# Kernel tuning notes

Hardware: AMD Instinct MI355X
Metric: run time of the kernel (lower is better)

The kernel has to match this reference:

```python
import jax, jax.numpy as jnp
import numpy as np

N_HEADS = 8
TOPK = 64
LN_EPS = 1e-5


def layernorm(x, g, b):
    mu = jnp.mean(x, axis=-1, keepdims=True)
    var = jnp.mean((x - mu) ** 2, axis=-1, keepdims=True)
    return (x - mu) * jax.lax.rsqrt(var + LN_EPS) * g + b


def mha(x, wq, wk, wv, wo, causal):
    # x: [B, S, H]; weights are torch nn.Linear style [out, in]
    B, S, H = x.shape
    hd = H // N_HEADS
    scale = 1.0 / np.sqrt(hd)

    def proj(w):
        return (x @ w.T).reshape(B, S, N_HEADS, hd).transpose(0, 2, 1, 3)  # [B, n, S, hd]

    q, k, v = proj(wq), proj(wk), proj(wv)
    s = jnp.einsum('bnqd,bnkd->bnqk', q, k) * scale
    if causal:
        m = jnp.tril(jnp.ones((S, S), bool))
        s = jnp.where(m, s, jnp.finfo(s.dtype).min)
    a = jax.nn.softmax(s, axis=-1)
    o = jnp.einsum('bnqk,bnkd->bnqd', a, v).transpose(0, 2, 1, 3).reshape(B, S, H)
    return o @ wo.T


def topk_activation(x, k):
    # x: [N, F]; keep top-k per row, zero elsewhere (matches topk + scatter_)
    vals, idx = jax.lax.top_k(x, k)
    rows = jnp.arange(x.shape[0])[:, None]
    return jnp.zeros_like(x).at[rows, idx].set(vals)


def setup_inputs() -> dict:
    key = jax.random.key(0)
    B, D, L, H, F = 8, 16, 128, 512, 4096
    ks = jax.random.split(key, 12)
    s = 1.0 / np.sqrt(H)
    w = lambda k, shp, sc: jax.random.normal(k, shp, jnp.float32) * sc
    return {
        'zL': w(ks[0], (B, D, L, H), 1.0),
        'wq_l': w(ks[1], (H, H), s), 'wk_l': w(ks[2], (H, H), s),
        'wv_l': w(ks[3], (H, H), s), 'wo_l': w(ks[4], (H, H), s),
        'gamma_l': jnp.ones(H, jnp.float32), 'beta_l': jnp.zeros(H, jnp.float32),
        'wq_d': w(ks[5], (H, H), s), 'wk_d': w(ks[6], (H, H), s),
        'wv_d': w(ks[7], (H, H), s), 'wo_d': w(ks[8], (H, H), s),
        'gamma_d': jnp.ones(H, jnp.float32), 'beta_d': jnp.zeros(H, jnp.float32),
        'dict_enc': w(ks[9], (F, H), np.sqrt(2.0 / (H + F))),
        'bias_pre': jnp.zeros(H, jnp.float32),
        'bias_enc': jnp.zeros(F, jnp.float32),
        'query_token': jnp.zeros(H, jnp.float32),
    }


def reference(zL, wq_l, wk_l, wv_l, wo_l, gamma_l, beta_l,
              wq_d, wk_d, wv_d, wo_d, gamma_d, beta_d,
              dict_enc, bias_pre, bias_enc, query_token):
    B, D, L, H = zL.shape
    F = dict_enc.shape[0]
    # prepend learned query token along depth, drop last layer
    qt = jnp.broadcast_to(query_token[None, None, None, :], (B, 1, L, H))
    x = jnp.concatenate([qt, zL[:, :-1, :, :]], axis=1)  # [B, D, L, H]
    # non-causal attention over L within each (b, d)
    x = x.reshape(B * D, L, H)
    x = x + mha(layernorm(x, gamma_l, beta_l), wq_l, wk_l, wv_l, wo_l, causal=False)
    # causal attention over D within each (b, l)
    x = x.reshape(B, D, L, H).transpose(0, 2, 1, 3).reshape(B * L, D, H)
    x = x + mha(layernorm(x, gamma_d, beta_d), wq_d, wk_d, wv_d, wo_d, causal=True)
    x_prior = x.reshape(B, L, D, H).transpose(0, 2, 1, 3)  # [B, D, L, H]
    # dictionary encode on residual (detached in original)
    N = B * D * L
    x_src = jax.lax.stop_gradient(zL - x_prior).reshape(N, H)
    logits = (x_src - bias_pre[None, :]) @ dict_enc.T + bias_enc
    z_dense = jax.nn.relu(logits)
    z_flat = topk_activation(z_dense, TOPK)
    z_n = z_flat.reshape(B, D, L, F)
    return z_n, x_prior
```

## Files before the change

kernel.cpp:

```cpp
#include <hip/hip_runtime.h>
#include <stdint.h>

#define NTOK 16384
#define HDIM 512
#define FDIM 4096
#define NHEAD 8

typedef __attribute__((ext_vector_type(8))) _Float16 f16x8;
typedef __attribute__((ext_vector_type(16))) float f32x16;
#define LOSCALE 4096.0f
#define LOINV   (1.0f / 4096.0f)

static __device__ __forceinline__ void ld8f(const float* p, float* v) {
    *(float4*)&v[0] = *(const float4*)p;
    *(float4*)&v[4] = *(const float4*)(p + 4);
}
static __device__ __forceinline__ void st8f(float* p, const float* v) {
    *(float4*)p       = *(const float4*)&v[0];
    *(float4*)(p + 4) = *(const float4*)&v[4];
}

__global__ __launch_bounds__(256) void build_x_k(const float* __restrict__ zL,
                                                 const float* __restrict__ qt,
                                                 float* __restrict__ X) {
    int idx = blockIdx.x * 256 + threadIdx.x;
    int n = idx >> 6;
    int h = (idx & 63) << 3;
    int d = (n >> 7) & 15;
    const float* src = d ? (zL + (((size_t)(n - 128)) << 9) + h) : (qt + h);
    float v[8];
    ld8f(src, v);
    st8f(X + (((size_t)n) << 9) + h, v);
}

__global__ __launch_bounds__(256) void ln_stats_k(const float* __restrict__ X,
                                                  float* __restrict__ mu,
                                                  float* __restrict__ rstd) {
    int row = blockIdx.x * 4 + (threadIdx.x >> 6);
    int lane = threadIdx.x & 63;
    const float* xr = X + (((size_t)row) << 9) + (lane << 3);
    float v[8];
    ld8f(xr, v);
    float s = 0.f;
#pragma unroll
    for (int i = 0; i < 8; ++i) s += v[i];
#pragma unroll
    for (int off = 32; off; off >>= 1) s += __shfl_xor(s, off);
    float m = s * (1.0f / 512.0f);
    float q = 0.f;
#pragma unroll
    for (int i = 0; i < 8; ++i) { float d = v[i] - m; q += d * d; }
#pragma unroll
    for (int off = 32; off; off >>= 1) q += __shfl_xor(q, off);
    if (lane == 0) {
        mu[row] = m;
        rstd[row] = 1.0f / sqrtf(q * (1.0f / 512.0f) + 1e-5f);
    }
}

template<bool LN, bool ADD_C, bool BIAS>
__global__ __launch_bounds__(256) void gemm_k(const float* __restrict__ A,
                                              const float* __restrict__ W,
                                              float* __restrict__ C,
                                              const float* __restrict__ mu,
                                              const float* __restrict__ rstd,
                                              const float* __restrict__ gamma,
                                              const float* __restrict__ beta,
                                              const float* __restrict__ bias,
                                              int M, int N, int K) {
    __shared__ float As[16][128];
    __shared__ float Bs[16][128];
    const int tid = threadIdx.x;
    const int bm = blockIdx.y << 7;
    const int bn = blockIdx.x << 7;
    const int tx = tid & 15, ty = tid >> 4;
    const int lr = tid >> 1;
    const int lk = (tid & 1) << 3;
    const float* Ap = A + (size_t)(bm + lr) * K + lk;
    const float* Wp = W + (size_t)(bn + lr) * K + lk;
    float mu_r = 0.f, rs_r = 0.f;
    if (LN) { mu_r = mu[bm + lr]; rs_r = rstd[bm + lr]; }
    float acc[8][8];
#pragma unroll
    for (int i = 0; i < 8; ++i)
#pragma unroll
        for (int j = 0; j < 8; ++j) acc[i][j] = 0.f;

    float av[8], bv[8];
    ld8f(Ap, av);
    ld8f(Wp, bv);
    if (LN) {
        float gv[8], be[8];
        ld8f(gamma + lk, gv);
        ld8f(beta + lk, be);
#pragma unroll
        for (int i = 0; i < 8; ++i) av[i] = (av[i] - mu_r) * rs_r * gv[i] + be[i];
    }
    const int nIt = K >> 4;
    for (int it = 0; it < nIt; ++it) {
        __syncthreads();
#pragma unroll
        for (int i = 0; i < 8; ++i) { As[lk + i][lr] = av[i]; Bs[lk + i][lr] = bv[i]; }
        __syncthreads();
        if (it + 1 < nIt) {
            const int k0 = (it + 1) << 4;
            ld8f(Ap + k0, av);
            ld8f(Wp + k0, bv);
            if (LN) {
                float gv[8], be[8];
                ld8f(gamma + k0 + lk, gv);
                ld8f(beta + k0 + lk, be);
#pragma unroll
                for (int i = 0; i < 8; ++i) av[i] = (av[i] - mu_r) * rs_r * gv[i] + be[i];
            }
        }
#pragma unroll
        for (int kk = 0; kk < 16; ++kk) {
            float a[8], b[8];
            *(float4*)&a[0] = *(const float4*)&As[kk][ty << 3];
            *(float4*)&a[4] = *(const float4*)&As[kk][(ty << 3) + 4];
            *(float4*)&b[0] = *(const float4*)&Bs[kk][tx << 3];
            *(float4*)&b[4] = *(const float4*)&Bs[kk][(tx << 3) + 4];
#pragma unroll
            for (int i = 0; i < 8; ++i)
#pragma unroll
                for (int j = 0; j < 8; ++j)
                    acc[i][j] = fmaf(a[i], b[j], acc[i][j]);
        }
    }
    const int orow = bm + (ty << 3);
    const int ocol = bn + (tx << 3);
    float badd[8];
    if (BIAS) ld8f(bias + ocol, badd);
#pragma unroll
    for (int i = 0; i < 8; ++i) {
        float* cp = C + (size_t)(orow + i) * N + ocol;
        float o[8];
#pragma unroll
        for (int j = 0; j < 8; ++j) o[j] = acc[i][j];
        if (BIAS) {
#pragma unroll
            for (int j = 0; j < 8; ++j) o[j] += badd[j];
        }
        if (ADD_C) {
            float4 c0 = *(const float4*)cp;
            float4 c1 = *(const float4*)(cp + 4);
            o[0] += c0.x; o[1] += c0.y; o[2] += c0.z; o[3] += c0.w;
            o[4] += c1.x; o[5] += c1.y; o[6] += c1.z; o[7] += c1.w;
        }
        *(float4*)cp       = make_float4(o[0], o[1], o[2], o[3]);
        *(float4*)(cp + 4) = make_float4(o[4], o[5], o[6], o[7]);
    }
}

__global__ __launch_bounds__(512) void attn_l_k(float* __restrict__ QO,
                                                const float* __restrict__ K,
                                                const float* __restrict__ V) {
    __shared__ float ks[128][64];
    __shared__ float vs[128][64];
    const int seq = blockIdx.x, head = blockIdx.y;
    const int t = threadIdx.x;
    const size_t base = (((size_t)seq) << 16) + (head << 6);
#pragma unroll
    for (int i = 0; i < 4; ++i) {
        int slot = t + (i << 9);
        int row = slot >> 4;
        int c4 = (slot & 15) << 2;
        size_t g = base + (((size_t)row) << 9) + c4;
        *(float4*)&ks[row][c4] = *(const float4*)(K + g);
        *(float4*)&vs[row][c4] = *(const float4*)(V + g);
    }
    __syncthreads();
    const int r = t >> 2;
    const int q16 = (t & 3) << 4;
    float* qp = QO + base + (((size_t)r) << 9) + q16;
    float qr[16];
#pragma unroll
    for (int i = 0; i < 4; ++i) *(float4*)&qr[i << 2] = *(const float4*)(qp + (i << 2));
    float o[16];
#pragma unroll
    for (int d = 0; d < 16; ++d) o[d] = 0.f;
    float m = -1e30f, l = 0.f;
    for (int j = 0; j < 128; ++j) {
        const float* kp = &ks[j][q16];
        float s0 = 0.f, s1 = 0.f, s2 = 0.f, s3 = 0.f;
#pragma unroll
        for (int d = 0; d < 16; d += 4) {
            s0 = fmaf(qr[d + 0], kp[d + 0], s0);
            s1 = fmaf(qr[d + 1], kp[d + 1], s1);
            s2 = fmaf(qr[d + 2], kp[d + 2], s2);
            s3 = fmaf(qr[d + 3], kp[d + 3], s3);
        }
        float sp = (s0 + s1) + (s2 + s3);
        sp += __shfl_xor(sp, 1);
        sp += __shfl_xor(sp, 2);
        float s = sp * 0.125f;
        if (s > m) {
            float c = expf(m - s);
#pragma unroll
            for (int d = 0; d < 16; ++d) o[d] *= c;
            l *= c;
            m = s;
        }
        float w = expf(s - m);
        l += w;
        const float* vp = &vs[j][q16];
#pragma unroll
        for (int d = 0; d < 16; ++d) o[d] = fmaf(w, vp[d], o[d]);
    }
    float inv = 1.0f / l;
#pragma unroll
    for (int i = 0; i < 4; ++i)
        *(float4*)(qp + (i << 2)) = make_float4(o[i * 4] * inv, o[i * 4 + 1] * inv,
                                                o[i * 4 + 2] * inv, o[i * 4 + 3] * inv);
}

__global__ __launch_bounds__(128) void attn_d_k(float* __restrict__ QO,
                                                const float* __restrict__ K,
                                                const float* __restrict__ V) {
    __shared__ float ks[16][512];
    __shared__ float vs[16][512];
    const int bl = blockIdx.x;
    const int b = bl >> 7, l = bl & 127;
    const int t = threadIdx.x;
    const size_t base = ((size_t)(b * 2048 + l)) << 9;
#pragma unroll
    for (int i = 0; i < 16; ++i) {
        int slot = t + (i << 7);
        int row = slot >> 7;
        int c4 = (slot & 127) << 2;
        size_t g = base + (((size_t)row) << 16) + c4;
        *(float4*)&ks[row][c4] = *(const float4*)(K + g);
        *(float4*)&vs[row][c4] = *(const float4*)(V + g);
    }
    __syncthreads();
    const int head = t >> 4, dr = t & 15;
    const int ho = head << 6;
    float qr[64];
    float* qp = QO + base + (((size_t)dr) << 16) + ho;
#pragma unroll
    for (int i = 0; i < 16; ++i) *(float4*)&qr[i << 2] = *(const float4*)(qp + (i << 2));
    float s[16];
    float m = -1e30f;
#pragma unroll
    for (int j = 0; j < 16; ++j) {
        float s0 = 0.f, s1 = 0.f, s2 = 0.f, s3 = 0.f;
#pragma unroll
        for (int d = 0; d < 64; d += 4) {
            s0 = fmaf(qr[d + 0], ks[j][ho + d + 0], s0);
            s1 = fmaf(qr[d + 1], ks[j][ho + d + 1], s1);
            s2 = fmaf(qr[d + 2], ks[j][ho + d + 2], s2);
            s3 = fmaf(qr[d + 3], ks[j][ho + d + 3], s3);
        }
        float sv = ((s0 + s1) + (s2 + s3)) * 0.125f;
        s[j] = (j <= dr) ? sv : -1e30f;
        m = fmaxf(m, s[j]);
    }
    float lsum = 0.f;
#pragma unroll
    for (int j = 0; j < 16; ++j) {
        float w = (j <= dr) ? expf(s[j] - m) : 0.f;
        s[j] = w;
        lsum += w;
    }
    float inv = 1.0f / lsum;
    float o[64];
#pragma unroll
    for (int d = 0; d < 64; ++d) o[d] = 0.f;
#pragma unroll
    for (int j = 0; j < 16; ++j) {
        float w = s[j];
#pragma unroll
        for (int d = 0; d < 64; ++d) o[d] = fmaf(w, vs[j][ho + d], o[d]);
    }
#pragma unroll
    for (int i = 0; i < 16; ++i)
        *(float4*)(qp + (i << 2)) = make_float4(o[i * 4] * inv, o[i * 4 + 1] * inv,
                                                o[i * 4 + 2] * inv, o[i * 4 + 3] * inv);
}

__global__ __launch_bounds__(256) void cast_out_k(const float* __restrict__ X,
                                                  float* __restrict__ out) {
    int idx = blockIdx.x * 256 + threadIdx.x;
    float v[8];
    ld8f(X + (((size_t)idx) << 3), v);
    st8f(out + (((size_t)idx) << 3), v);
}

__global__ __launch_bounds__(256) void xsrc_k(const float* __restrict__ zL,
                                              const float* __restrict__ bias_pre,
                                              float* __restrict__ X) {
    int idx = blockIdx.x * 256 + threadIdx.x;
    int h = (idx & 63) << 3;
    float z[8], p[8], x[8];
    ld8f(zL + (((size_t)idx) << 3), z);
    ld8f(bias_pre + h, p);
    float* xp = X + (((size_t)idx) << 3);
    ld8f(xp, x);
    float o[8];
#pragma unroll
    for (int i = 0; i < 8; ++i) o[i] = z[i] - x[i] - p[i];
    st8f(xp, o);
}

__global__ __launch_bounds__(256) void xprior_xsrc_k(const float* __restrict__ zL,
                                                     const float* __restrict__ bias_pre,
                                                     float* __restrict__ X,
                                                     float* __restrict__ out_xp) {
    int idx = blockIdx.x * 256 + threadIdx.x;
    int h = (idx & 63) << 3;
    float z[8], p[8], x[8];
    ld8f(zL + (((size_t)idx) << 3), z);
    ld8f(bias_pre + h, p);
    float* xp = X + (((size_t)idx) << 3);
    ld8f(xp, x);
    st8f(out_xp + (((size_t)idx) << 3), x);
    float o[8];
#pragma unroll
    for (int i = 0; i < 8; ++i) o[i] = z[i] - x[i] - p[i];
    st8f(xp, o);
}

__global__ __launch_bounds__(256) void split2_k(const float* __restrict__ in,
                                                _Float16* __restrict__ ph,
                                                _Float16* __restrict__ pl) {
    int idx = blockIdx.x * 256 + threadIdx.x;
    float v[8];
    ld8f(in + (((size_t)idx) << 3), v);
    _Float16 h8[8], l8[8];
#pragma unroll
    for (int i = 0; i < 8; ++i) {
        _Float16 h = (_Float16)v[i];
        float r = v[i] - (float)h;
        h8[i] = h;
        l8[i] = (_Float16)(r * LOSCALE);
    }
    *(int4*)(ph + (((size_t)idx) << 3)) = *(int4*)h8;
    *(int4*)(pl + (((size_t)idx) << 3)) = *(int4*)l8;
}

__global__ __launch_bounds__(256) void split2_ln_k(const float* __restrict__ X,
                                                   const float* __restrict__ mu,
                                                   const float* __restrict__ rstd,
                                                   const float* __restrict__ gamma,
                                                   const float* __restrict__ beta,
                                                   _Float16* __restrict__ ph,
                                                   _Float16* __restrict__ pl) {
    int idx = blockIdx.x * 256 + threadIdx.x;
    int row = idx >> 6;
    int h = (idx & 63) << 3;
    float v[8], gv[8], be[8];
    ld8f(X + (((size_t)idx) << 3), v);
    ld8f(gamma + h, gv);
    ld8f(beta + h, be);
    float m = mu[row], rs = rstd[row];
    _Float16 h8[8], l8[8];
#pragma unroll
    for (int i = 0; i < 8; ++i) {
        float y = (v[i] - m) * rs * gv[i] + be[i];
        _Float16 hh = (_Float16)y;
        float r = y - (float)hh;
        h8[i] = hh;
        l8[i] = (_Float16)(r * LOSCALE);
    }
    *(int4*)(ph + (((size_t)idx) << 3)) = *(int4*)h8;
    *(int4*)(pl + (((size_t)idx) << 3)) = *(int4*)l8;
}

#define LDT 36
template<bool ADD_C, bool BIAS>
__global__ __launch_bounds__(256) void gemm_f16_k(
        const _Float16* __restrict__ Xh, const _Float16* __restrict__ Xl,
        const _Float16* __restrict__ Wh, const _Float16* __restrict__ Wl,
        const float* __restrict__ bias, float* __restrict__ Cout, int ldc) {
    __shared__ _Float16 Ah[128][LDT], Al[128][LDT];
    __shared__ _Float16 Bh[128][LDT], Bl[128][LDT];
    const int tid = threadIdx.x;
    const int bm = blockIdx.y << 7, bn = blockIdx.x << 7;
    const int w = tid >> 6, lane = tid & 63;
    const int wr = w >> 1, wc = w & 1;
    const int l31 = lane & 31, hh = lane >> 5;
    f32x16 acc1[2][2], acc2[2][2];
#pragma unroll
    for (int i = 0; i < 2; ++i)
#pragma unroll
        for (int j = 0; j < 2; ++j)
#pragma unroll
            for (int r = 0; r < 16; ++r) { acc1[i][j][r] = 0.f; acc2[i][j][r] = 0.f; }

    for (int k0 = 0; k0 < HDIM; k0 += 32) {
        __syncthreads();
#pragma unroll
        for (int i = 0; i < 2; ++i) {
            int s = tid + (i << 8);
            int row = s >> 2, kg = (s & 3) << 3;
            size_t ga = (size_t)(bm + row) * HDIM + k0 + kg;
            size_t gb = (size_t)(bn + row) * HDIM + k0 + kg;
            *(int4*)&Ah[row][kg] = *(const int4*)(Xh + ga);
            *(int4*)&Al[row][kg] = *(const int4*)(Xl + ga);
            *(int4*)&Bh[row][kg] = *(const int4*)(Wh + gb);
            *(int4*)&Bl[row][kg] = *(const int4*)(Wl + gb);
        }
        __syncthreads();
#pragma unroll
        for (int kh = 0; kh < 2; ++kh) {
            const int ko = (kh << 4) + (hh << 3);
            f16x8 fah[2], fal[2];
#pragma unroll
            for (int mf = 0; mf < 2; ++mf) {
                int ar = (wr << 6) + (mf << 5) + l31;
                fah[mf] = *(const f16x8*)&Ah[ar][ko];
                fal[mf] = *(const f16x8*)&Al[ar][ko];
            }
#pragma unroll
            for (int nf = 0; nf < 2; ++nf) {
                int bc_ = (wc << 6) + (nf << 5) + l31;
                f16x8 bh = *(const f16x8*)&Bh[bc_][ko];
                f16x8 bl = *(const f16x8*)&Bl[bc_][ko];
#pragma unroll
                for (int mf = 0; mf < 2; ++mf) {
                    acc1[mf][nf] = __builtin_amdgcn_mfma_f32_32x32x16_f16(fah[mf], bh, acc1[mf][nf], 0, 0, 0);
                    acc2[mf][nf] = __builtin_amdgcn_mfma_f32_32x32x16_f16(fah[mf], bl, acc2[mf][nf], 0, 0, 0);
                    acc2[mf][nf] = __builtin_amdgcn_mfma_f32_32x32x16_f16(fal[mf], bh, acc2[mf][nf], 0, 0, 0);
                }
            }
        }
    }
#pragma unroll
    for (int mf = 0; mf < 2; ++mf)
#pragma unroll
        for (int nf = 0; nf < 2; ++nf) {
            int col = bn + (wc << 6) + (nf << 5) + l31;
            float badd = BIAS ? bias[col] : 0.f;
#pragma unroll
            for (int r = 0; r < 16; ++r) {
                int row = bm + (wr << 6) + (mf << 5) + (r & 3) + ((r >> 2) << 3) + (hh << 2);
                float* cp = Cout + (size_t)row * ldc + col;
                float val = acc1[mf][nf][r] + acc2[mf][nf][r] * LOINV + badd;
                if (ADD_C) val += *cp;
                *cp = val;
            }
        }
}

__global__ __launch_bounds__(256) void topk_k(const float* __restrict__ logits,
                                              float* __restrict__ out) {
    const int row = blockIdx.x;
    const float* lr = logits + (((size_t)row) << 12);
    const int t = threadIdx.x;
    float v[16]; uint32_t u[16];
#pragma unroll
    for (int i = 0; i < 16; ++i) {
        float x = fmaxf(lr[t + (i << 8)], 0.f);
        v[i] = x;
        u[i] = __float_as_uint(x);
    }
    __shared__ int red[4];
    __shared__ unsigned long long bits[64];
    __shared__ int s_cut;
    uint32_t prefix = 0;
    bool exact = false;
    for (int bit = 30; bit >= 0; --bit) {
        uint32_t c = prefix | (1u << bit);
        int cnt = 0;
#pragma unroll
        for (int i = 0; i < 16; ++i) cnt += (u[i] >= c) ? 1 : 0;
#pragma unroll
        for (int off = 32; off; off >>= 1) cnt += __shfl_xor(cnt, off);
        if ((t & 63) == 0) red[t >> 6] = cnt;
        __syncthreads();
        int total = red[0] + red[1] + red[2] + red[3];
        __syncthreads();
        if (total >= 64) prefix = c;
        if (total == 64) { exact = true; break; }
    }
    float* orow = out + (((size_t)row) << 12);
    if (exact) {
#pragma unroll
        for (int i = 0; i < 16; ++i) {
            int col = t + (i << 8);
            orow[col] = (u[i] >= prefix) ? v[i] : 0.f;
        }
        return;
    }
    const uint32_t T64 = prefix;
    int cg = 0;
#pragma unroll
    for (int i = 0; i < 16; ++i) cg += (u[i] > T64) ? 1 : 0;
#pragma unroll
    for (int off = 32; off; off >>= 1) cg += __shfl_xor(cg, off);
    if ((t & 63) == 0) red[t >> 6] = cg;
    __syncthreads();
    const int ngt = red[0] + red[1] + red[2] + red[3];
    int cut = -1;
    if (T64 != 0u) {
        const int r = 64 - ngt;
        if (t < 64) bits[t] = 0ull;
        __syncthreads();
#pragma unroll
        for (int i = 0; i < 16; ++i) {
            if (u[i] == T64) {
                int col = t + (i << 8);
                atomicOr(&bits[col >> 6], 1ull << (col & 63));
            }
        }
        __syncthreads();
        if (t == 0) {
            int need = r, cs = FDIM - 1;
            for (int wd = 0; wd < 64; ++wd) {
                int pc = __popcll(bits[wd]);
                if (need <= pc) {
                    unsigned long long bb = bits[wd];
                    for (int q = 1; q < need; ++q) bb &= bb - 1;
                    cs = (wd << 6) + (__ffsll(bb) - 1);
                    break;
                }
                need -= pc;
            }
            s_cut = cs;
        }
        __syncthreads();
        cut = s_cut;
    }
#pragma unroll
    for (int i = 0; i < 16; ++i) {
        int col = t + (i << 8);
        bool keep = (u[i] > T64) || (T64 != 0u && u[i] == T64 && col <= cut);
        orow[col] = keep ? v[i] : 0.f;
    }
}

extern "C" void kernel_launch(void* const* d_in, const int* in_sizes, int n_in,
                              void* d_out, int out_size, void* d_ws, size_t ws_size,
                              hipStream_t stream) {
    const float* zL      = (const float*)d_in[0];
    const float* gamma_l = (const float*)d_in[5];
    const float* beta_l  = (const float*)d_in[6];
    const float* gamma_d = (const float*)d_in[11];
    const float* beta_d  = (const float*)d_in[12];
    const float* dict_e  = (const float*)d_in[13];
    const float* bias_pre= (const float*)d_in[14];
    const float* bias_enc= (const float*)d_in[15];
    const float* qt      = (const float*)d_in[16];
    const float* wproj[8] = { (const float*)d_in[1], (const float*)d_in[2],
                              (const float*)d_in[3], (const float*)d_in[4],
                              (const float*)d_in[7], (const float*)d_in[8],
                              (const float*)d_in[9], (const float*)d_in[10] };

    float* out_z  = (float*)d_out;
    float* out_xp = out_z + (size_t)NTOK * FDIM;

    const size_t NHf = (size_t)NTOK * HDIM;
    float* B0 = (float*)d_out;
    float* B1 = B0 + NHf;
    float* B2 = B1 + NHf;
    float* B3 = B2 + NHf;

    float* wsf    = (float*)d_ws;
    float* mu     = wsf + 64;
    float* rstd   = mu + NTOK;
    float* logits = rstd + NTOK;

    const size_t dictE = (size_t)FDIM * HDIM;
    const size_t WE    = (size_t)HDIM * HDIM;

    int crows = NTOK;
    const size_t mfmaFixedB = (64 + 2 * (size_t)NTOK) * sizeof(float)
                            + (2 * dictE + 16 * WE + 2 * NHf) * sizeof(_Float16);
    while (crows > 128 &&
           mfmaFixedB + (size_t)crows * FDIM * sizeof(float) > ws_size) crows >>= 1;
    const bool use_mfma_proj =
        mfmaFixedB + (size_t)crows * FDIM * sizeof(float) <= ws_size;

    const dim3 blk256(256), blk128(128), blk512(512);
    const dim3 gElem(4096);
    const dim3 gProjM(HDIM / 128, NTOK / 128);

    if (use_mfma_proj) {
        _Float16* dh = (_Float16*)(logits + (size_t)crows * FDIM);
        _Float16* dl = dh + dictE;
        _Float16* wsp = dh + 2 * dictE;
        _Float16* xh = wsp + 16 * WE;
        _Float16* xl = xh + NHf;
        _Float16* wh[8], *wl[8];
        for (int i = 0; i < 8; ++i) {
            wh[i] = wsp + (size_t)i * 2 * WE;
            wl[i] = wh[i] + WE;
        }

        for (int i = 0; i < 8; ++i)
            split2_k<<<dim3(WE / 8 / 256), blk256, 0, stream>>>(wproj[i], wh[i], wl[i]);
        split2_k<<<dim3(dictE / 8 / 256), blk256, 0, stream>>>(dict_e, dh, dl);

        build_x_k<<<gElem, blk256, 0, stream>>>(zL, qt, B0);

        ln_stats_k<<<dim3(NTOK / 4), blk256, 0, stream>>>(B0, mu, rstd);
        split2_ln_k<<<gElem, blk256, 0, stream>>>(B0, mu, rstd, gamma_l, beta_l, xh, xl);
        gemm_f16_k<false, false><<<gProjM, blk256, 0, stream>>>(xh, xl, wh[0], wl[0], nullptr, B1, HDIM);
        gemm_f16_k<false, false><<<gProjM, blk256, 0, stream>>>(xh, xl, wh[1], wl[1], nullptr, B2, HDIM);
        gemm_f16_k<false, false><<<gProjM, blk256, 0, stream>>>(xh, xl, wh[2], wl[2], nullptr, B3, HDIM);
        attn_l_k<<<dim3(128, NHEAD), blk512, 0, stream>>>(B1, B2, B3);
        split2_k<<<gElem, blk256, 0, stream>>>(B1, xh, xl);
        gemm_f16_k<true, false><<<gProjM, blk256, 0, stream>>>(xh, xl, wh[3], wl[3], nullptr, B0, HDIM);

        ln_stats_k<<<dim3(NTOK / 4), blk256, 0, stream>>>(B0, mu, rstd);
        split2_ln_k<<<gElem, blk256, 0, stream>>>(B0, mu, rstd, gamma_d, beta_d, xh, xl);
        gemm_f16_k<false, false><<<gProjM, blk256, 0, stream>>>(xh, xl, wh[4], wl[4], nullptr, B1, HDIM);
        gemm_f16_k<false, false><<<gProjM, blk256, 0, stream>>>(xh, xl, wh[5], wl[5], nullptr, B2, HDIM);
        gemm_f16_k<false, false><<<gProjM, blk256, 0, stream>>>(xh, xl, wh[6], wl[6], nullptr, B3, HDIM);
        attn_d_k<<<dim3(1024), blk128, 0, stream>>>(B1, B2, B3);
        split2_k<<<gElem, blk256, 0, stream>>>(B1, xh, xl);
        gemm_f16_k<true, false><<<gProjM, blk256, 0, stream>>>(xh, xl, wh[7], wl[7], nullptr, B0, HDIM);

        xprior_xsrc_k<<<gElem, blk256, 0, stream>>>(zL, bias_pre, B0, out_xp);
        split2_k<<<gElem, blk256, 0, stream>>>(B0, xh, xl);

        const dim3 gDict(FDIM / 128, crows / 128);
        for (int c0 = 0; c0 < NTOK; c0 += crows) {
            gemm_f16_k<false, true><<<gDict, blk256, 0, stream>>>(
                xh + (size_t)c0 * HDIM, xl + (size_t)c0 * HDIM,
                dh, dl, bias_enc, logits, FDIM);
            topk_k<<<dim3(crows), blk256, 0, stream>>>(logits, out_z + (size_t)c0 * FDIM);
        }
    } else {
        int cr = 2048;
        const size_t fixedB = (64 + 2 * (size_t)NTOK) * sizeof(float) + dictE * 2 * sizeof(_Float16);
        while (cr > 128 &&
               fixedB + (size_t)cr * FDIM * sizeof(float) + (size_t)cr * HDIM * 2 * sizeof(_Float16) > ws_size)
            cr >>= 1;
        _Float16* dh = (_Float16*)(logits + (size_t)cr * FDIM);
        _Float16* dl = dh + dictE;
        _Float16* xh = dl + dictE;
        _Float16* xl = xh + (size_t)cr * HDIM;

        build_x_k<<<gElem, blk256, 0, stream>>>(zL, qt, B0);
        ln_stats_k<<<dim3(NTOK / 4), blk256, 0, stream>>>(B0, mu, rstd);
        gemm_k<true,  false, false><<<gProjM, blk256, 0, stream>>>(B0, wproj[0], B1, mu, rstd, gamma_l, beta_l, nullptr, NTOK, HDIM, HDIM);
        gemm_k<true,  false, false><<<gProjM, blk256, 0, stream>>>(B0, wproj[1], B2, mu, rstd, gamma_l, beta_l, nullptr, NTOK, HDIM, HDIM);
        gemm_k<true,  false, false><<<gProjM, blk256, 0, stream>>>(B0, wproj[2], B3, mu, rstd, gamma_l, beta_l, nullptr, NTOK, HDIM, HDIM);
        attn_l_k<<<dim3(128, NHEAD), blk512, 0, stream>>>(B1, B2, B3);
        gemm_k<false, true,  false><<<gProjM, blk256, 0, stream>>>(B1, wproj[3], B0, nullptr, nullptr, nullptr, nullptr, nullptr, NTOK, HDIM, HDIM);
        ln_stats_k<<<dim3(NTOK / 4), blk256, 0, stream>>>(B0, mu, rstd);
        gemm_k<true,  false, false><<<gProjM, blk256, 0, stream>>>(B0, wproj[4], B1, mu, rstd, gamma_d, beta_d, nullptr, NTOK, HDIM, HDIM);
        gemm_k<true,  false, false><<<gProjM, blk256, 0, stream>>>(B0, wproj[5], B2, mu, rstd, gamma_d, beta_d, nullptr, NTOK, HDIM, HDIM);
        gemm_k<true,  false, false><<<gProjM, blk256, 0, stream>>>(B0, wproj[6], B3, mu, rstd, gamma_d, beta_d, nullptr, NTOK, HDIM, HDIM);
        attn_d_k<<<dim3(1024), blk128, 0, stream>>>(B1, B2, B3);
        gemm_k<false, true,  false><<<gProjM, blk256, 0, stream>>>(B1, wproj[7], B0, nullptr, nullptr, nullptr, nullptr, nullptr, NTOK, HDIM, HDIM);
        cast_out_k<<<gElem, blk256, 0, stream>>>(B0, out_xp);
        xsrc_k<<<gElem, blk256, 0, stream>>>(zL, bias_pre, B0);
        split2_k<<<dim3(dictE / 8 / 256), blk256, 0, stream>>>(dict_e, dh, dl);
        const dim3 gDict(FDIM / 128, cr / 128);
        for (int c0 = NTOK - cr; c0 >= 0; c0 -= cr) {
            split2_k<<<dim3(cr * HDIM / 8 / 256), blk256, 0, stream>>>(B0 + (size_t)c0 * HDIM, xh, xl);
            gemm_f16_k<false, true><<<gDict, blk256, 0, stream>>>(xh, xl, dh, dl, bias_enc, logits, FDIM);
            topk_k<<<dim3(cr), blk256, 0, stream>>>(logits, out_z + (size_t)c0 * FDIM);
        }
    }
}
```

Before: 1.193 ms.

## Shrink MFMA GEMM tile to 128x64 and route fallback projections through MFMA

The split-fp16 MFMA GEMM tile drops from 128x128 to 128x64 output, so each wave holds half as many accumulators and the grids get twice as many blocks. The LDS row pad changes from 36 to 34. The fallback path, used when the workspace is small, swaps its scalar fp32 GEMMs for the split-fp16 MFMA GEMM with chunked input splitting, and fuses the output copy with the residual subtract. The aim is higher occupancy and more parallel blocks; the cost is lower per-block data reuse and possible LDS bank conflicts from the new pad.

```diff
diff --git a/kernel.cpp b/kernel.cpp
--- a/kernel.cpp
+++ b/kernel.cpp
@@ -58,101 +58,6 @@
     }
 }
 
-template<bool LN, bool ADD_C, bool BIAS>
-__global__ __launch_bounds__(256) void gemm_k(const float* __restrict__ A,
-                                              const float* __restrict__ W,
-                                              float* __restrict__ C,
-                                              const float* __restrict__ mu,
-                                              const float* __restrict__ rstd,
-                                              const float* __restrict__ gamma,
-                                              const float* __restrict__ beta,
-                                              const float* __restrict__ bias,
-                                              int M, int N, int K) {
-    __shared__ float As[16][128];
-    __shared__ float Bs[16][128];
-    const int tid = threadIdx.x;
-    const int bm = blockIdx.y << 7;
-    const int bn = blockIdx.x << 7;
-    const int tx = tid & 15, ty = tid >> 4;
-    const int lr = tid >> 1;
-    const int lk = (tid & 1) << 3;
-    const float* Ap = A + (size_t)(bm + lr) * K + lk;
-    const float* Wp = W + (size_t)(bn + lr) * K + lk;
-    float mu_r = 0.f, rs_r = 0.f;
-    if (LN) { mu_r = mu[bm + lr]; rs_r = rstd[bm + lr]; }
-    float acc[8][8];
-#pragma unroll
-    for (int i = 0; i < 8; ++i)
-#pragma unroll
-        for (int j = 0; j < 8; ++j) acc[i][j] = 0.f;
-
-    float av[8], bv[8];
-    ld8f(Ap, av);
-    ld8f(Wp, bv);
-    if (LN) {
-        float gv[8], be[8];
-        ld8f(gamma + lk, gv);
-        ld8f(beta + lk, be);
-#pragma unroll
-        for (int i = 0; i < 8; ++i) av[i] = (av[i] - mu_r) * rs_r * gv[i] + be[i];
-    }
-    const int nIt = K >> 4;
-    for (int it = 0; it < nIt; ++it) {
-        __syncthreads();
-#pragma unroll
-        for (int i = 0; i < 8; ++i) { As[lk + i][lr] = av[i]; Bs[lk + i][lr] = bv[i]; }
-        __syncthreads();
-        if (it + 1 < nIt) {
-            const int k0 = (it + 1) << 4;
-            ld8f(Ap + k0, av);
-            ld8f(Wp + k0, bv);
-            if (LN) {
-                float gv[8], be[8];
-                ld8f(gamma + k0 + lk, gv);
-                ld8f(beta + k0 + lk, be);
-#pragma unroll
-                for (int i = 0; i < 8; ++i) av[i] = (av[i] - mu_r) * rs_r * gv[i] + be[i];
-            }
-        }
-#pragma unroll
-        for (int kk = 0; kk < 16; ++kk) {
-            float a[8], b[8];
-            *(float4*)&a[0] = *(const float4*)&As[kk][ty << 3];
-            *(float4*)&a[4] = *(const float4*)&As[kk][(ty << 3) + 4];
-            *(float4*)&b[0] = *(const float4*)&Bs[kk][tx << 3];
-            *(float4*)&b[4] = *(const float4*)&Bs[kk][(tx << 3) + 4];
-#pragma unroll
-            for (int i = 0; i < 8; ++i)
-#pragma unroll
-                for (int j = 0; j < 8; ++j)
-                    acc[i][j] = fmaf(a[i], b[j], acc[i][j]);
-        }
-    }
-    const int orow = bm + (ty << 3);
-    const int ocol = bn + (tx << 3);
-    float badd[8];
-    if (BIAS) ld8f(bias + ocol, badd);
-#pragma unroll
-    for (int i = 0; i < 8; ++i) {
-        float* cp = C + (size_t)(orow + i) * N + ocol;
-        float o[8];
-#pragma unroll
-        for (int j = 0; j < 8; ++j) o[j] = acc[i][j];
-        if (BIAS) {
-#pragma unroll
-            for (int j = 0; j < 8; ++j) o[j] += badd[j];
-        }
-        if (ADD_C) {
-            float4 c0 = *(const float4*)cp;
-            float4 c1 = *(const float4*)(cp + 4);
-            o[0] += c0.x; o[1] += c0.y; o[2] += c0.z; o[3] += c0.w;
-            o[4] += c1.x; o[5] += c1.y; o[6] += c1.z; o[7] += c1.w;
-        }
-        *(float4*)cp       = make_float4(o[0], o[1], o[2], o[3]);
-        *(float4*)(cp + 4) = make_float4(o[4], o[5], o[6], o[7]);
-    }
-}
-
 __global__ __launch_bounds__(512) void attn_l_k(float* __restrict__ QO,
                                                 const float* __restrict__ K,
                                                 const float* __restrict__ V) {
@@ -277,30 +182,6 @@
     for (int i = 0; i < 16; ++i)
         *(float4*)(qp + (i << 2)) = make_float4(o[i * 4] * inv, o[i * 4 + 1] * inv,
                                                 o[i * 4 + 2] * inv, o[i * 4 + 3] * inv);
-}
-
-__global__ __launch_bounds__(256) void cast_out_k(const float* __restrict__ X,
-                                                  float* __restrict__ out) {
-    int idx = blockIdx.x * 256 + threadIdx.x;
-    float v[8];
-    ld8f(X + (((size_t)idx) << 3), v);
-    st8f(out + (((size_t)idx) << 3), v);
-}
-
-__global__ __launch_bounds__(256) void xsrc_k(const float* __restrict__ zL,
-                                              const float* __restrict__ bias_pre,
-                                              float* __restrict__ X) {
-    int idx = blockIdx.x * 256 + threadIdx.x;
-    int h = (idx & 63) << 3;
-    float z[8], p[8], x[8];
-    ld8f(zL + (((size_t)idx) << 3), z);
-    ld8f(bias_pre + h, p);
-    float* xp = X + (((size_t)idx) << 3);
-    ld8f(xp, x);
-    float o[8];
-#pragma unroll
-    for (int i = 0; i < 8; ++i) o[i] = z[i] - x[i] - p[i];
-    st8f(xp, o);
 }
 
 __global__ __launch_bounds__(256) void xprior_xsrc_k(const float* __restrict__ zL,
@@ -367,26 +248,25 @@
     *(int4*)(pl + (((size_t)idx) << 3)) = *(int4*)l8;
 }
 
-#define LDT 36
+#define LDT 34
 template<bool ADD_C, bool BIAS>
 __global__ __launch_bounds__(256) void gemm_f16_k(
         const _Float16* __restrict__ Xh, const _Float16* __restrict__ Xl,
         const _Float16* __restrict__ Wh, const _Float16* __restrict__ Wl,
         const float* __restrict__ bias, float* __restrict__ Cout, int ldc) {
     __shared__ _Float16 Ah[128][LDT], Al[128][LDT];
-    __shared__ _Float16 Bh[128][LDT], Bl[128][LDT];
+    __shared__ _Float16 Bh[64][LDT],  Bl[64][LDT];
     const int tid = threadIdx.x;
-    const int bm = blockIdx.y << 7, bn = blockIdx.x << 7;
+    const int bm = blockIdx.y << 7;
+    const int bn = blockIdx.x << 6;
     const int w = tid >> 6, lane = tid & 63;
     const int wr = w >> 1, wc = w & 1;
     const int l31 = lane & 31, hh = lane >> 5;
-    f32x16 acc1[2][2], acc2[2][2];
+    f32x16 acc1[2], acc2[2];
 #pragma unroll
     for (int i = 0; i < 2; ++i)
 #pragma unroll
-        for (int j = 0; j < 2; ++j)
-#pragma unroll
-            for (int r = 0; r < 16; ++r) { acc1[i][j][r] = 0.f; acc2[i][j][r] = 0.f; }
+        for (int r = 0; r < 16; ++r) { acc1[i][r] = 0.f; acc2[i][r] = 0.f; }
 
     for (int k0 = 0; k0 < HDIM; k0 += 32) {
         __syncthreads();
@@ -395,9 +275,12 @@
             int s = tid + (i << 8);
             int row = s >> 2, kg = (s & 3) << 3;
             size_t ga = (size_t)(bm + row) * HDIM + k0 + kg;
-            size_t gb = (size_t)(bn + row) * HDIM + k0 + kg;
             *(int4*)&Ah[row][kg] = *(const int4*)(Xh + ga);
             *(int4*)&Al[row][kg] = *(const int4*)(Xl + ga);
+        }
+        {
+            int row = tid >> 2, kg = (tid & 3) << 3;
+            size_t gb = (size_t)(bn + row) * HDIM + k0 + kg;
             *(int4*)&Bh[row][kg] = *(const int4*)(Wh + gb);
             *(int4*)&Bl[row][kg] = *(const int4*)(Wl + gb);
         }
@@ -412,35 +295,30 @@
                 fah[mf] = *(const f16x8*)&Ah[ar][ko];
                 fal[mf] = *(const f16x8*)&Al[ar][ko];
             }
-#pragma unroll
-            for (int nf = 0; nf < 2; ++nf) {
-                int bc_ = (wc << 6) + (nf << 5) + l31;
-                f16x8 bh = *(const f16x8*)&Bh[bc_][ko];
-                f16x8 bl = *(const f16x8*)&Bl[bc_][ko];
-#pragma unroll
-                for (int mf = 0; mf < 2; ++mf) {
-                    acc1[mf][nf] = __builtin_amdgcn_mfma_f32_32x32x16_f16(fah[mf], bh, acc1[mf][nf], 0, 0, 0);
-                    acc2[mf][nf] = __builtin_amdgcn_mfma_f32_32x32x16_f16(fah[mf], bl, acc2[mf][nf], 0, 0, 0);
-                    acc2[mf][nf] = __builtin_amdgcn_mfma_f32_32x32x16_f16(fal[mf], bh, acc2[mf][nf], 0, 0, 0);
-                }
+            int bc_ = (wc << 5) + l31;
+            f16x8 bh = *(const f16x8*)&Bh[bc_][ko];
+            f16x8 bl = *(const f16x8*)&Bl[bc_][ko];
+#pragma unroll
+            for (int mf = 0; mf < 2; ++mf) {
+                acc1[mf] = __builtin_amdgcn_mfma_f32_32x32x16_f16(fah[mf], bh, acc1[mf], 0, 0, 0);
+                acc2[mf] = __builtin_amdgcn_mfma_f32_32x32x16_f16(fah[mf], bl, acc2[mf], 0, 0, 0);
+                acc2[mf] = __builtin_amdgcn_mfma_f32_32x32x16_f16(fal[mf], bh, acc2[mf], 0, 0, 0);
             }
         }
     }
-#pragma unroll
-    for (int mf = 0; mf < 2; ++mf)
-#pragma unroll
-        for (int nf = 0; nf < 2; ++nf) {
-            int col = bn + (wc << 6) + (nf << 5) + l31;
-            float badd = BIAS ? bias[col] : 0.f;
-#pragma unroll
-            for (int r = 0; r < 16; ++r) {
-                int row = bm + (wr << 6) + (mf << 5) + (r & 3) + ((r >> 2) << 3) + (hh << 2);
-                float* cp = Cout + (size_t)row * ldc + col;
-                float val = acc1[mf][nf][r] + acc2[mf][nf][r] * LOINV + badd;
-                if (ADD_C) val += *cp;
-                *cp = val;
-            }
-        }
+    const int col = bn + (wc << 5) + l31;
+    const float badd = BIAS ? bias[col] : 0.f;
+#pragma unroll
+    for (int mf = 0; mf < 2; ++mf) {
+#pragma unroll
+        for (int r = 0; r < 16; ++r) {
+            int row = bm + (wr << 6) + (mf << 5) + (r & 3) + ((r >> 2) << 3) + (hh << 2);
+            float* cp = Cout + (size_t)row * ldc + col;
+            float val = acc1[mf][r] + acc2[mf][r] * LOINV + badd;
+            if (ADD_C) val += *cp;
+            *cp = val;
+        }
+    }
 }
 
 __global__ __launch_bounds__(256) void topk_k(const float* __restrict__ logits,
@@ -569,14 +447,13 @@
                             + (2 * dictE + 16 * WE + 2 * NHf) * sizeof(_Float16);
     while (crows > 128 &&
            mfmaFixedB + (size_t)crows * FDIM * sizeof(float) > ws_size) crows >>= 1;
-    const bool use_mfma_proj =
-        mfmaFixedB + (size_t)crows * FDIM * sizeof(float) <= ws_size;
+    const bool ok = mfmaFixedB + (size_t)128 * FDIM * sizeof(float) <= ws_size;
 
     const dim3 blk256(256), blk128(128), blk512(512);
     const dim3 gElem(4096);
-    const dim3 gProjM(HDIM / 128, NTOK / 128);
-
-    if (use_mfma_proj) {
+    const dim3 gProjM(HDIM / 64, NTOK / 128);
+
+    if (ok) {
         _Float16* dh = (_Float16*)(logits + (size_t)crows * FDIM);
         _Float16* dl = dh + dictE;
         _Float16* wsp = dh + 2 * dictE;
@@ -615,7 +492,7 @@
         xprior_xsrc_k<<<gElem, blk256, 0, stream>>>(zL, bias_pre, B0, out_xp);
         split2_k<<<gElem, blk256, 0, stream>>>(B0, xh, xl);
 
-        const dim3 gDict(FDIM / 128, crows / 128);
+        const dim3 gDict(FDIM / 64, crows / 128);
         for (int c0 = 0; c0 < NTOK; c0 += crows) {
             gemm_f16_k<false, true><<<gDict, blk256, 0, stream>>>(
                 xh + (size_t)c0 * HDIM, xl + (size_t)c0 * HDIM,
@@ -626,33 +503,59 @@
         int cr = 2048;
         const size_t fixedB = (64 + 2 * (size_t)NTOK) * sizeof(float) + dictE * 2 * sizeof(_Float16);
         while (cr > 128 &&
-               fixedB + (size_t)cr * FDIM * sizeof(float) + (size_t)cr * HDIM * 2 * sizeof(_Float16) > ws_size)
+               fixedB + (size_t)cr * FDIM * sizeof(float) + ((size_t)cr * HDIM + 16 * WE) * 2 * sizeof(_Float16) > ws_size)
             cr >>= 1;
         _Float16* dh = (_Float16*)(logits + (size_t)cr * FDIM);
         _Float16* dl = dh + dictE;
         _Float16* xh = dl + dictE;
         _Float16* xl = xh + (size_t)cr * HDIM;
+        _Float16* wh = xl + (size_t)cr * HDIM;
+        _Float16* wlo = wh + WE;
 
         build_x_k<<<gElem, blk256, 0, stream>>>(zL, qt, B0);
+
         ln_stats_k<<<dim3(NTOK / 4), blk256, 0, stream>>>(B0, mu, rstd);
-        gemm_k<true,  false, false><<<gProjM, blk256, 0, stream>>>(B0, wproj[0], B1, mu, rstd, gamma_l, beta_l, nullptr, NTOK, HDIM, HDIM);
-        gemm_k<true,  false, false><<<gProjM, blk256, 0, stream>>>(B0, wproj[1], B2, mu, rstd, gamma_l, beta_l, nullptr, NTOK, HDIM, HDIM);
-        gemm_k<true,  false, false><<<gProjM, blk256, 0, stream>>>(B0, wproj[2], B3, mu, rstd, gamma_l, beta_l, nullptr, NTOK, HDIM, HDIM);
+        for (int i = 0; i < 3; ++i) {
+            split2_k<<<dim3(WE / 8 / 256), blk256, 0, stream>>>(wproj[i], wh, wlo);
+            float* dst = (i == 0) ? B1 : (i == 1) ? B2 : B3;
+            for (int c0 = 0; c0 < NTOK; c0 += cr) {
+                split2_ln_k<<<dim3(cr * HDIM / 8 / 256), blk256, 0, stream>>>(
+                    B0 + (size_t)c0 * HDIM, mu + c0, rstd + c0, gamma_l, beta_l, xh, xl);
+                gemm_f16_k<false, false><<<dim3(HDIM / 64, cr / 128), blk256, 0, stream>>>(
+                    xh, xl, wh, wlo, nullptr, dst + (size_t)c0 * HDIM, HDIM);
+            }
+        }
         attn_l_k<<<dim3(128, NHEAD), blk512, 0, stream>>>(B1, B2, B3);
-        gemm_k<false, true,  false><<<gProjM, blk256, 0, stream>>>(B1, wproj[3], B0, nullptr, nullptr, nullptr, nullptr, nullptr, NTOK, HDIM, HDIM);
+        split2_k<<<dim3(WE / 8 / 256), blk256, 0, stream>>>(wproj[3], wh, wlo);
+        for (int c0 = 0; c0 < NTOK; c0 += cr) {
+            split2_k<<<dim3(cr * HDIM / 8 / 256), blk256, 0, stream>>>(B1 + (size_t)c0 * HDIM, xh, xl);
+            gemm_f16_k<true, false><<<dim3(HDIM / 64, cr / 128), blk256, 0, stream>>>(
+                xh, xl, wh, wlo, nullptr, B0 + (size_t)c0 * HDIM, HDIM);
+        }
         ln_stats_k<<<dim3(NTOK / 4), blk256, 0, stream>>>(B0, mu, rstd);
-        gemm_k<true,  false, false><<<gProjM, blk256, 0, stream>>>(B0, wproj[4], B1, mu, rstd, gamma_d, beta_d, nullptr, NTOK, HDIM, HDIM);
-        gemm_k<true,  false, false><<<gProjM, blk256, 0, stream>>>(B0, wproj[5], B2, mu, rstd, gamma_d, beta_d, nullptr, NTOK, HDIM, HDIM);
-        gemm_k<true,  false, false><<<gProjM, blk256, 0, stream>>>(B0, wproj[6], B3, mu, rstd, gamma_d, beta_d, nullptr, NTOK, HDIM, HDIM);
+        for (int i = 4; i < 7; ++i) {
+            split2_k<<<dim3(WE / 8 / 256), blk256, 0, stream>>>(wproj[i], wh, wlo);
+            float* dst = (i == 4) ? B1 : (i == 5) ? B2 : B3;
+            for (int c0 = 0; c0 < NTOK; c0 += cr) {
+                split2_ln_k<<<dim3(cr * HDIM / 8 / 256), blk256, 0, stream>>>(
+                    B0 + (size_t)c0 * HDIM, mu + c0, rstd + c0, gamma_d, beta_d, xh, xl);
+                gemm_f16_k<false, false><<<dim3(HDIM / 64, cr / 128), blk256, 0, stream>>>(
+                    xh, xl, wh, wlo, nullptr, dst + (size_t)c0 * HDIM, HDIM);
+            }
+        }
         attn_d_k<<<dim3(1024), blk128, 0, stream>>>(B1, B2, B3);
-        gemm_k<false, true,  false><<<gProjM, blk256, 0, stream>>>(B1, wproj[7], B0, nullptr, nullptr, nullptr, nullptr, nullptr, NTOK, HDIM, HDIM);
-        cast_out_k<<<gElem, blk256, 0, stream>>>(B0, out_xp);
-        xsrc_k<<<gElem, blk256, 0, stream>>>(zL, bias_pre, B0);
+        split2_k<<<dim3(WE / 8 / 256), blk256, 0, stream>>>(wproj[7], wh, wlo);
+        for (int c0 = 0; c0 < NTOK; c0 += cr) {
+            split2_k<<<dim3(cr * HDIM / 8 / 256), blk256, 0, stream>>>(B1 + (size_t)c0 * HDIM, xh, xl);
+            gemm_f16_k<true, false><<<dim3(HDIM / 64, cr / 128), blk256, 0, stream>>>(
+                xh, xl, wh, wlo, nullptr, B0 + (size_t)c0 * HDIM, HDIM);
+        }
+        xprior_xsrc_k<<<gElem, blk256, 0, stream>>>(zL, bias_pre, B0, out_xp);
         split2_k<<<dim3(dictE / 8 / 256), blk256, 0, stream>>>(dict_e, dh, dl);
-        const dim3 gDict(FDIM / 128, cr / 128);
         for (int c0 = NTOK - cr; c0 >= 0; c0 -= cr) {
             split2_k<<<dim3(cr * HDIM / 8 / 256), blk256, 0, stream>>>(B0 + (size_t)c0 * HDIM, xh, xl);
-            gemm_f16_k<false, true><<<gDict, blk256, 0, stream>>>(xh, xl, dh, dl, bias_enc, logits, FDIM);
+            gemm_f16_k<false, true><<<dim3(FDIM / 64, cr / 128), blk256, 0, stream>>>(
+                xh, xl, dh, dl, bias_enc, logits, FDIM);
             topk_k<<<dim3(cr), blk256, 0, stream>>>(logits, out_z + (size_t)c0 * FDIM);
         }
     }
```

Result: faster. 1.168 ms (-2.1%).
